# Optimization experiments

Measured on AMD Instinct MI355X. Metric: run time of the kernel, lower is better.

Reference implementation:

```python
import jax, jax.numpy as jnp
import numpy as np

N = 100000
E = 1600000
C_IN = 32
C_OUT = 64
DIM = 3
K = 2 ** DIM  # kernel_size=2 per pseudo-dim, degree=1 => 8 kernel slots
EPS = 1e-5

_BITS = jnp.asarray(np.array([[(c >> d) & 1 for d in range(DIM)] for c in range(K)], dtype=np.float32))  # [K,DIM]


def spline_basis(edge_attr):
    # edge_attr: [E,DIM] pseudo coords in [0,1]. kernel_size=2, degree=1 =>
    # per-dim linear basis (1-u, u); product over dims gives [E,K].
    u = edge_attr[:, None, :]            # [E,1,DIM]
    b = _BITS[None, :, :]                # [1,K,DIM]
    return jnp.prod(b * u + (1.0 - b) * (1.0 - u), axis=-1)  # [E,K]


def spline_conv(x, edge_index, edge_attr, W, W_root):
    # SplineConv with aggr='mean', root_weight=True, bias=False.
    src, dst = edge_index[0], edge_index[1]
    basis = spline_basis(edge_attr)                      # [E,K]
    x_j = x[src]                                         # [E,C_in] gather
    msg = jnp.einsum('ek,ei,kio->eo', basis, x_j, W)     # [E,C_out]
    agg = jax.ops.segment_sum(msg, dst, num_segments=N)  # [N,C_out] scatter-add
    cnt = jax.ops.segment_sum(jnp.ones((msg.shape[0],), msg.dtype), dst, num_segments=N)
    agg = agg / jnp.maximum(cnt, 1.0)[:, None]           # mean aggregation
    return agg + x @ W_root


def batch_norm(x, gamma, beta):
    mu = jnp.mean(x, axis=0)
    var = jnp.var(x, axis=0)
    return (x - mu) * jax.lax.rsqrt(var + EPS) * gamma + beta


def setup_inputs() -> dict:
    key = jax.random.key(0)
    ks = jax.random.split(key, 12)
    x = jax.random.normal(ks[0], (N, C_IN), jnp.float32)
    edge_index = jax.random.randint(ks[1], (2, E), 0, N, jnp.int32)
    edge_attr = jax.random.uniform(ks[2], (E, DIM), jnp.float32)
    s1 = 1.0 / np.sqrt(C_IN)
    s2 = 1.0 / np.sqrt(C_OUT)
    return {
        'x': x,
        'edge_index': edge_index,
        'edge_attr': edge_attr,
        'W1': jax.random.normal(ks[3], (K, C_IN, C_OUT), jnp.float32) * s1,
        'root1': jax.random.normal(ks[4], (C_IN, C_OUT), jnp.float32) * s1,
        'g1': jnp.ones((C_OUT,), jnp.float32),
        'b1': jnp.zeros((C_OUT,), jnp.float32),
        'W2': jax.random.normal(ks[5], (K, C_OUT, C_OUT), jnp.float32) * s2,
        'root2': jax.random.normal(ks[6], (C_OUT, C_OUT), jnp.float32) * s2,
        'g2': jnp.ones((C_OUT,), jnp.float32),
        'b2': jnp.zeros((C_OUT,), jnp.float32),
        'W_skip': jax.random.normal(ks[7], (C_IN, C_OUT), jnp.float32) * s1,
        'g_skip': jnp.ones((C_OUT,), jnp.float32),
        'b_skip': jnp.zeros((C_OUT,), jnp.float32),
    }


def reference(x, edge_index, edge_attr, W1, root1, g1, b1, W2, root2, g2, b2, W_skip, g_skip, b_skip):
    # ConvBlock: SplineConv -> BN -> elu
    h = spline_conv(x, edge_index, edge_attr, W1, root1)
    h = jax.nn.elu(batch_norm(h, g1, b1))
    # ConvBlockWithSkip: SplineConv -> BN; Linear skip -> BN; elu(sum)
    skip = batch_norm(x @ W_skip, g_skip, b_skip)
    h2 = batch_norm(spline_conv(h, edge_index, edge_attr, W2, root2), g2, b2)
    return jax.nn.elu(h2 + skip)
```

## Files before the change

### kernel.cpp

```cpp
#include <hip/hip_runtime.h>
#include <cstdint>

#define BN_EPS 1e-5f

typedef __attribute__((ext_vector_type(8))) short bf16x8;
typedef __attribute__((ext_vector_type(4))) float f32x4;
typedef unsigned int uint32;
typedef unsigned short u16;

__device__ inline u16 f2bf(float f) {
  unsigned int b = __float_as_uint(f);
  b += 0x7FFFu + ((b >> 16) & 1u);
  return (u16)(b >> 16);
}
__device__ inline float bf2f(u16 u) { return __uint_as_float((unsigned int)u << 16); }

__global__ void pack_bt(const float* __restrict__ W1, const float* __restrict__ root1,
                        const float* __restrict__ Wskip, const float* __restrict__ W2,
                        const float* __restrict__ root2, u16* __restrict__ B1t,
                        u16* __restrict__ B2t) {
  int idx = blockIdx.x * 256 + threadIdx.x;
  if (idx < 128 * 288) {
    int n = idx / 288, a = idx % 288;
    float v;
    if (a < 256) {
      int i = a >> 3, k = a & 7;
      v = (n < 64) ? W1[k * 2048 + i * 64 + n] : 0.f;
    } else {
      int i = a - 256;
      v = (n < 64) ? root1[i * 64 + n] : Wskip[i * 64 + (n - 64)];
    }
    B1t[idx] = f2bf(v);
  } else {
    int j = idx - 128 * 288;
    if (j < 64 * 576) {
      int n = j / 576, a = j % 576;
      float v;
      if (a < 512) {
        int i = a >> 3, k = a & 7;
        v = W2[k * 4096 + i * 64 + n];
      } else {
        v = root2[(a - 512) * 64 + n];
      }
      B2t[j] = f2bf(v);
    }
  }
}

__global__ __launch_bounds__(256) void conv_x(const float* __restrict__ x,
                                              u16* __restrict__ xbf, int total8) {
  int i = blockIdx.x * 256 + threadIdx.x;
  if (i >= total8) return;
  const float4* xp = (const float4*)x;
  float4 a = xp[2 * i], b = xp[2 * i + 1];
  union { u16 s[8]; uint4 u; } p;
  p.s[0] = f2bf(a.x); p.s[1] = f2bf(a.y); p.s[2] = f2bf(a.z); p.s[3] = f2bf(a.w);
  p.s[4] = f2bf(b.x); p.s[5] = f2bf(b.y); p.s[6] = f2bf(b.z); p.s[7] = f2bf(b.w);
  ((uint4*)xbf)[i] = p.u;
}

__global__ void hist_dst(const int* __restrict__ ei, int E, int* __restrict__ indeg) {
  int e = blockIdx.x * 256 + threadIdx.x;
  if (e >= E) return;
  atomicAdd(&indeg[ei[E + e]], 1);
}

__global__ __launch_bounds__(1024) void scan_block(const int* __restrict__ in,
                                                   int* __restrict__ part,
                                                   int* __restrict__ bsum, int N) {
  __shared__ int tmp[1024];
  int i = blockIdx.x * 1024 + threadIdx.x;
  int v = (i < N) ? in[i] : 0;
  tmp[threadIdx.x] = v;
  __syncthreads();
  for (int ofs = 1; ofs < 1024; ofs <<= 1) {
    int t = (threadIdx.x >= (unsigned)ofs) ? tmp[threadIdx.x - ofs] : 0;
    __syncthreads();
    tmp[threadIdx.x] += t;
    __syncthreads();
  }
  if (i < N) part[i] = tmp[threadIdx.x] - v;
  if (threadIdx.x == 1023) bsum[blockIdx.x] = tmp[1023];
}

__global__ __launch_bounds__(1024) void scan_top(int* __restrict__ bsum, int nb) {
  __shared__ int tmp[1024];
  int v = (threadIdx.x < (unsigned)nb) ? bsum[threadIdx.x] : 0;
  tmp[threadIdx.x] = v;
  __syncthreads();
  for (int ofs = 1; ofs < 1024; ofs <<= 1) {
    int t = (threadIdx.x >= (unsigned)ofs) ? tmp[threadIdx.x - ofs] : 0;
    __syncthreads();
    tmp[threadIdx.x] += t;
    __syncthreads();
  }
  if (threadIdx.x < (unsigned)nb) bsum[threadIdx.x] = tmp[threadIdx.x] - v;
}

__global__ void scan_add(const int* __restrict__ part, const int* __restrict__ bsum,
                         int* __restrict__ rowptr, int* __restrict__ cursor, int N, int E) {
  int i = blockIdx.x * 256 + threadIdx.x;
  if (i < N) {
    int r = part[i] + bsum[i >> 10];
    rowptr[i] = r;
    cursor[i] = r;
  }
  if (i == 0) rowptr[N] = E;
}

__global__ void edge_scatter(const int* __restrict__ ei, const float* __restrict__ attr, int E,
                             int* __restrict__ cursor, uint4* __restrict__ emeta) {
  int e = blockIdx.x * 256 + threadIdx.x;
  if (e >= E) return;
  int src = ei[e], dst = ei[E + e];
  float u0 = attr[3 * e + 0], u1 = attr[3 * e + 1], u2 = attr[3 * e + 2];
  float p0 = 1.f - u0, p1 = 1.f - u1, p2 = 1.f - u2;
  float w00 = p1 * p2, w10 = u1 * p2, w01 = p1 * u2, w11 = u1 * u2;
  float w[8] = {p0 * w00, u0 * w00, p0 * w10, u0 * w10,
                p0 * w01, u0 * w01, p0 * w11, u0 * w11};
  union { _Float16 h[8]; uint32 u[4]; } pk;
#pragma unroll
  for (int j = 0; j < 8; j++) pk.h[j] = (_Float16)w[j];
  int pos = atomicAdd(&cursor[dst], 1);
  emeta[2 * (size_t)pos + 0] = make_uint4((uint32)src, 0u, pk.u[0], pk.u[1]);
  emeta[2 * (size_t)pos + 1] = make_uint4(pk.u[2], pk.u[3], 0u, 0u);
}

template <int PC>
__device__ inline void sc_gather(const u16* __restrict__ tab, int src, int p, float* xf) {
  if (PC == 1) {
    xf[0] = bf2f(tab[(size_t)src * 32 + p]);
  } else {
    uint32 u = *(const uint32*)(tab + (size_t)src * 64 + 2 * p);
    xf[0] = __uint_as_float(u << 16);
    xf[1] = __uint_as_float(u & 0xFFFF0000u);
  }
}

template <int PC>
__device__ inline void sc_fma(float* acc, uint4 m0, uint4 m1, const float* xf) {
  union { uint32 u[4]; _Float16 h[8]; } w;
  w.u[0] = m0.z; w.u[1] = m0.w; w.u[2] = m1.x; w.u[3] = m1.y;
#pragma unroll
  for (int k = 0; k < 8; k++) {
    float wk = (float)w.h[k];
#pragma unroll
    for (int c = 0; c < PC; c++) acc[k * PC + c] += wk * xf[c];
  }
}

template <int PC>
__global__ __launch_bounds__(256) void msg_accum(const u16* __restrict__ tab,
                                                 const int* __restrict__ rowptr,
                                                 const uint4* __restrict__ emeta,
                                                 int n0, int n1, u16* __restrict__ T) {
  const int tid = threadIdx.x;
  const int lane = tid & 63;
  const int wv = tid >> 6;
  const int nwaves = gridDim.x * 4;
  const int p = lane & 31;
  const int eh = lane >> 5;

  for (int n = n0 + blockIdx.x * 4 + wv; n < n1; n += nwaves) {
    const int e0 = __builtin_amdgcn_readfirstlane(rowptr[n]);
    const int e1 = __builtin_amdgcn_readfirstlane(rowptr[n + 1]);
    float acc[8 * PC];
#pragma unroll
    for (int j = 0; j < 8 * PC; j++) acc[j] = 0.f;

    int e = e0;
    for (; e + 4 <= e1; e += 4) {
      const size_t iA = 2 * (size_t)(e + eh);
      const size_t iB = 2 * (size_t)(e + 2 + eh);
      uint4 a0 = emeta[iA], a1 = emeta[iA + 1];
      uint4 b0 = emeta[iB], b1 = emeta[iB + 1];
      float xa[PC], xb[PC];
      sc_gather<PC>(tab, (int)a0.x, p, xa);
      sc_gather<PC>(tab, (int)b0.x, p, xb);
      sc_fma<PC>(acc, a0, a1, xa);
      sc_fma<PC>(acc, b0, b1, xb);
    }
    for (; e < e1; e += 2) {
      int ee = e + eh;
      bool act = ee < e1;
      if (!act) ee = e;
      const size_t i0 = 2 * (size_t)ee;
      uint4 m0 = emeta[i0], m1 = emeta[i0 + 1];
      float xv[PC];
      sc_gather<PC>(tab, (int)m0.x, p, xv);
      if (!act) {
#pragma unroll
        for (int c = 0; c < PC; c++) xv[c] = 0.f;
      }
      sc_fma<PC>(acc, m0, m1, xv);
    }

#pragma unroll
    for (int j = 0; j < 8 * PC; j++) acc[j] += __shfl_xor(acc[j], 32);

    float inv = 1.f / fmaxf((float)(e1 - e0), 1.f);
    if (eh == 0) {
      u16* rowp = T + (size_t)(n - n0) * (256 * PC);
#pragma unroll
      for (int c = 0; c < PC; c++) {
        union { u16 s[8]; uint4 u; } pk;
#pragma unroll
        for (int k = 0; k < 8; k++) pk.s[k] = f2bf(acc[k * PC + c] * inv);
        *(uint4*)(rowp + ((size_t)(PC * p + c)) * 8) = pk.u;
      }
    }
  }
}

template <int KT, int KX, int NC>
__global__ __launch_bounds__(256) void gemm_agg(const u16* __restrict__ T,
                                                const u16* __restrict__ X,
                                                const u16* __restrict__ Bt,
                                                u16* __restrict__ O1, u16* __restrict__ O2,
                                                int rowOff, int rows) {
  const int K = KT + KX;
  const int tid = threadIdx.x;
  const int lane = tid & 63;
  const int wv = tid >> 6;
  const int rowbase = blockIdx.x * 64 + wv * 16;
  const int m = lane & 15;
  const int quad = lane >> 4;
  const int k0 = quad * 8;

  int ar = rowbase + m;
  if (ar > rows - 1) ar = rows - 1;

  bf16x8 afrag[K / 32];
#pragma unroll
  for (int f = 0; f < K / 32; f++) {
    if (f * 32 < KT)
      afrag[f] = *(const bf16x8*)(T + (size_t)ar * KT + f * 32 + k0);
    else
      afrag[f] = *(const bf16x8*)(X + (size_t)(rowOff + ar) * KX + (f * 32 - KT) + k0);
  }

  for (int col0 = 0; col0 < NC; col0 += 16) {
    f32x4 acc = {0.f, 0.f, 0.f, 0.f};
#pragma unroll
    for (int f = 0; f < K / 32; f++) {
      bf16x8 bfrag = *(const bf16x8*)(Bt + (size_t)(col0 + m) * K + f * 32 + k0);
      acc = __builtin_amdgcn_mfma_f32_16x16x32_bf16(afrag[f], bfrag, acc, 0, 0, 0);
    }
    const int col = col0 + m;
#pragma unroll
    for (int r = 0; r < 4; r++) {
      int gr = rowbase + quad * 4 + r;
      if (gr < rows) {
        size_t g = (size_t)(rowOff + gr);
        u16 v = f2bf(acc[r]);
        if (NC == 64 || col < 64) O1[g * 64 + col] = v;
        else O2[g * 64 + (col - 64)] = v;
      }
    }
  }
}

__global__ __launch_bounds__(256) void stats_k(const u16* __restrict__ A,
                                               const u16* __restrict__ B, int N,
                                               double* __restrict__ sums) {
  const int tid = threadIdx.x;
  const int c = tid & 63;
  const int wh = (tid >> 6) & 1;
  const int rep = tid >> 7;
  const u16* P = wh ? B : A;
  float s = 0.f, s2 = 0.f;
  if (P) {
    for (int n = blockIdx.x * 2 + rep; n < N; n += gridDim.x * 2) {
      float v = bf2f(P[(size_t)n * 64 + c]);
      s += v;
      s2 += v * v;
    }
  }
  __shared__ float red[256];
  red[tid] = s;
  __syncthreads();
  float t1 = (tid < 128) ? red[tid] + red[tid + 128] : 0.f;
  __syncthreads();
  red[tid] = s2;
  __syncthreads();
  if (tid < 128 && P) {
    float t2 = red[tid] + red[tid + 128];
    atomicAdd(&sums[wh * 128 + c], (double)t1);
    atomicAdd(&sums[wh * 128 + 64 + c], (double)t2);
  }
}

__global__ void bn_finalize2(const double* __restrict__ sums, const float* __restrict__ gA,
                             const float* __restrict__ bA, const float* __restrict__ gB,
                             const float* __restrict__ bB, float* __restrict__ scales, int N) {
  int t = threadIdx.x;
  int set = t >> 6, ch = t & 63;
  if (set == 1 && gB == nullptr) return;
  const float* g = set ? gB : gA;
  const float* b = set ? bB : bA;
  double mean = sums[set * 128 + ch] / (double)N;
  double var = sums[set * 128 + 64 + ch] / (double)N - mean * mean;
  double inv = 1.0 / sqrt(var + (double)BN_EPS);
  float sc = (float)((double)g[ch] * inv);
  scales[set * 128 + ch] = sc;
  scales[set * 128 + 64 + ch] = b[ch] - (float)mean * sc;
}

__global__ __launch_bounds__(256) void bn_elu_inplace(u16* __restrict__ h,
                                                      const float* __restrict__ sc, int total) {
  int idx = blockIdx.x * 256 + threadIdx.x;
  if (idx >= total) return;
  int ch = idx & 63;
  float v = bf2f(h[idx]) * sc[ch] + sc[64 + ch];
  v = v > 0.f ? v : expm1f(v);
  h[idx] = f2bf(v);
}

__global__ __launch_bounds__(256) void final_k(const u16* __restrict__ h2pre,
                                               const u16* __restrict__ skip,
                                               const float* __restrict__ sc2,
                                               const float* __restrict__ scS,
                                               float* __restrict__ out, int total) {
  int idx = blockIdx.x * 256 + threadIdx.x;
  if (idx >= total) return;
  int ch = idx & 63;
  float h2 = bf2f(h2pre[idx]) * sc2[ch] + sc2[64 + ch];
  float s = bf2f(skip[idx]) * scS[ch] + scS[64 + ch];
  float v = h2 + s;
  out[idx] = v > 0.f ? v : expm1f(v);
}

extern "C" void kernel_launch(void* const* d_in, const int* in_sizes, int n_in,
                              void* d_out, int out_size, void* d_ws, size_t ws_size,
                              hipStream_t stream) {
  const float* x     = (const float*)d_in[0];
  const int*   ei    = (const int*)d_in[1];
  const float* attr  = (const float*)d_in[2];
  const float* W1    = (const float*)d_in[3];
  const float* root1 = (const float*)d_in[4];
  const float* g1    = (const float*)d_in[5];
  const float* b1    = (const float*)d_in[6];
  const float* W2    = (const float*)d_in[7];
  const float* root2 = (const float*)d_in[8];
  const float* g2    = (const float*)d_in[9];
  const float* b2    = (const float*)d_in[10];
  const float* Wskip = (const float*)d_in[11];
  const float* gS    = (const float*)d_in[12];
  const float* bS    = (const float*)d_in[13];
  const int N = in_sizes[0] / 32;
  const int E = in_sizes[1] / 2;
  const int Nh = (N + 1) / 2;
  float* out = (float*)d_out;

  char* ws = (char*)d_ws;
  size_t off = 0;
  auto alloc = [&](size_t bytes) {
    void* p = ws + off;
    off = (off + bytes + 255) & ~(size_t)255;
    return p;
  };
  u16* B1t = (u16*)alloc(128 * 288 * 2);
  u16* B2t = (u16*)alloc(64 * 576 * 2);
  double* sums = (double*)alloc(6 * 64 * 8);
  float* scales = (float*)alloc(6 * 64 * 4);
  int* indeg = (int*)alloc((size_t)N * 4);
  int* rowptr = (int*)alloc(((size_t)N + 1) * 4);
  int* cursor = (int*)alloc((size_t)N * 4);
  int* bsum = (int*)alloc(1024 * 4);
  uint4* emeta = (uint4*)alloc((size_t)E * 32);
  u16* xbf = (u16*)alloc((size_t)N * 32 * 2);
  u16* T = (u16*)alloc((size_t)(N + 2) * 256 * 2);
  u16* h1 = (u16*)alloc((size_t)N * 64 * 2);
  u16* skip = (u16*)alloc((size_t)N * 64 * 2);
  u16* h2 = (u16*)alloc((size_t)N * 64 * 2);
  if (off > ws_size) return;

  hipMemsetAsync(indeg, 0, (size_t)N * 4, stream);
  hipMemsetAsync(sums, 0, 6 * 64 * 8, stream);

  pack_bt<<<(128 * 288 + 64 * 576 + 255) / 256, 256, 0, stream>>>(W1, root1, Wskip, W2, root2,
                                                                  B1t, B2t);
  conv_x<<<(N * 4 + 255) / 256, 256, 0, stream>>>(x, xbf, N * 4);

  const int eblocks = (E + 255) / 256;
  const int nb = (N + 1023) / 1024;
  hist_dst<<<eblocks, 256, 0, stream>>>(ei, E, indeg);
  scan_block<<<nb, 1024, 0, stream>>>(indeg, cursor, bsum, N);
  scan_top<<<1, 1024, 0, stream>>>(bsum, nb);
  scan_add<<<(N + 255) / 256, 256, 0, stream>>>(cursor, bsum, rowptr, indeg, N, E);
  edge_scatter<<<eblocks, 256, 0, stream>>>(ei, attr, E, indeg, emeta);

  msg_accum<1><<<2048, 256, 0, stream>>>(xbf, rowptr, emeta, 0, N, T);
  gemm_agg<256, 32, 128><<<(N + 63) / 64, 256, 0, stream>>>(T, xbf, B1t, h1, skip, 0, N);
  stats_k<<<512, 256, 0, stream>>>(h1, skip, N, sums);
  bn_finalize2<<<1, 128, 0, stream>>>(sums, g1, b1, gS, bS, scales, N);
  bn_elu_inplace<<<(N * 64 + 255) / 256, 256, 0, stream>>>(h1, scales, N * 64);

  for (int cph = 0; cph < 2; cph++) {
    int r0 = cph ? Nh : 0;
    int r1 = cph ? N : Nh;
    msg_accum<2><<<2048, 256, 0, stream>>>(h1, rowptr, emeta, r0, r1, T);
    gemm_agg<512, 64, 64><<<(r1 - r0 + 63) / 64, 256, 0, stream>>>(T, h1, B2t, h2, nullptr,
                                                                   r0, r1 - r0);
  }
  stats_k<<<512, 256, 0, stream>>>(h2, nullptr, N, sums + 4 * 64);
  bn_finalize2<<<1, 64, 0, stream>>>(sums + 4 * 64, g2, b2, nullptr, nullptr,
                                     scales + 4 * 64, N);

  final_k<<<(N * 64 + 255) / 256, 256, 0, stream>>>(h2, skip, scales + 4 * 64,
                                                    scales + 2 * 64, out, N * 64);
}
```

Baseline: 642.0 us.

## Two-pass bucketed edge scatter with per-XCD staging to localize CSR writes

Replaces the direct edge scatter with two passes. The first appends compact edge records into per-(dst bucket, XCD) staging slots, reusing the T buffer, and falls back to a direct scatter on overflow. The second kernel, one block per 256-node bucket, places the records into the CSR metadata, so the random 32-byte writes and cursor atomics land in a localized region. This costs an extra kernel pass, extra staging traffic and atomics, and reads a hardware register to get the XCD id.

```diff
diff --git a/kernel.cpp b/kernel.cpp
--- a/kernel.cpp
+++ b/kernel.cpp
@@ -14,6 +14,24 @@
   return (u16)(b >> 16);
 }
 __device__ inline float bf2f(u16 u) { return __uint_as_float((unsigned int)u << 16); }
+
+__device__ inline int get_xcd() {
+  uint32 x;
+  asm volatile("s_getreg_b32 %0, hwreg(HW_REG_XCC_ID)" : "=s"(x));
+  return (int)(x & 7u);
+}
+
+__device__ inline void make_w8(float u0, float u1, float u2, uint32* wu) {
+  float p0 = 1.f - u0, p1 = 1.f - u1, p2 = 1.f - u2;
+  float w00 = p1 * p2, w10 = u1 * p2, w01 = p1 * u2, w11 = u1 * u2;
+  float w[8] = {p0 * w00, u0 * w00, p0 * w10, u0 * w10,
+                p0 * w01, u0 * w01, p0 * w11, u0 * w11};
+  union { _Float16 h[8]; uint32 u[4]; } pk;
+#pragma unroll
+  for (int j = 0; j < 8; j++) pk.h[j] = (_Float16)w[j];
+#pragma unroll
+  for (int j = 0; j < 4; j++) wu[j] = pk.u[j];
+}
 
 __global__ void pack_bt(const float* __restrict__ W1, const float* __restrict__ root1,
                         const float* __restrict__ Wskip, const float* __restrict__ W2,
@@ -108,22 +126,53 @@
   if (i == 0) rowptr[N] = E;
 }
 
-__global__ void edge_scatter(const int* __restrict__ ei, const float* __restrict__ attr, int E,
-                             int* __restrict__ cursor, uint4* __restrict__ emeta) {
+__global__ __launch_bounds__(256) void stage_append(const int* __restrict__ ei,
+                                                    const float* __restrict__ attr, int E,
+                                                    int* __restrict__ bcnt,
+                                                    uint4* __restrict__ stage, int sbcap,
+                                                    int* __restrict__ cursor,
+                                                    uint4* __restrict__ emeta) {
   int e = blockIdx.x * 256 + threadIdx.x;
   if (e >= E) return;
   int src = ei[e], dst = ei[E + e];
   float u0 = attr[3 * e + 0], u1 = attr[3 * e + 1], u2 = attr[3 * e + 2];
-  float p0 = 1.f - u0, p1 = 1.f - u1, p2 = 1.f - u2;
-  float w00 = p1 * p2, w10 = u1 * p2, w01 = p1 * u2, w11 = u1 * u2;
-  float w[8] = {p0 * w00, u0 * w00, p0 * w10, u0 * w10,
-                p0 * w01, u0 * w01, p0 * w11, u0 * w11};
-  union { _Float16 h[8]; uint32 u[4]; } pk;
-#pragma unroll
-  for (int j = 0; j < 8; j++) pk.h[j] = (_Float16)w[j];
-  int pos = atomicAdd(&cursor[dst], 1);
-  emeta[2 * (size_t)pos + 0] = make_uint4((uint32)src, 0u, pk.u[0], pk.u[1]);
-  emeta[2 * (size_t)pos + 1] = make_uint4(pk.u[2], pk.u[3], 0u, 0u);
+  union { _Float16 h[2]; uint32 u; } y, z;
+  y.h[0] = (_Float16)u0; y.h[1] = (_Float16)u1;
+  z.h[0] = (_Float16)u2; z.h[1] = (_Float16)0.f;
+  int sb = (dst >> 8) * 8 + get_xcd();
+  int c = atomicAdd(&bcnt[sb], 1);
+  if (c < sbcap) {
+    stage[(size_t)sb * sbcap + c] = make_uint4((uint32)src, (uint32)dst, y.u, z.u);
+  } else {
+    uint32 wu[4];
+    make_w8((float)y.h[0], (float)y.h[1], (float)z.h[0], wu);
+    int pos = atomicAdd(&cursor[dst], 1);
+    emeta[2 * (size_t)pos + 0] = make_uint4((uint32)src, 0u, wu[0], wu[1]);
+    emeta[2 * (size_t)pos + 1] = make_uint4(wu[2], wu[3], 0u, 0u);
+  }
+}
+
+__global__ __launch_bounds__(256) void bucket_place(const uint4* __restrict__ stage,
+                                                    const int* __restrict__ bcnt, int sbcap,
+                                                    int* __restrict__ cursor,
+                                                    uint4* __restrict__ emeta) {
+  int b = blockIdx.x;
+  for (int xc = 0; xc < 8; xc++) {
+    int sb = b * 8 + xc;
+    int cnt = bcnt[sb];
+    if (cnt > sbcap) cnt = sbcap;
+    const uint4* sp = stage + (size_t)sb * sbcap;
+    for (int i = threadIdx.x; i < cnt; i += 256) {
+      uint4 r = sp[i];
+      union { uint32 u; _Float16 h[2]; } cy, cz;
+      cy.u = r.z; cz.u = r.w;
+      uint32 wu[4];
+      make_w8((float)cy.h[0], (float)cy.h[1], (float)cz.h[0], wu);
+      int pos = atomicAdd(&cursor[(int)r.y], 1);
+      emeta[2 * (size_t)pos + 0] = make_uint4(r.x, 0u, wu[0], wu[1]);
+      emeta[2 * (size_t)pos + 1] = make_uint4(wu[2], wu[3], 0u, 0u);
+    }
+  }
 }
 
 template <int PC>
@@ -352,6 +401,12 @@
   const int Nh = (N + 1) / 2;
   float* out = (float*)d_out;
 
+  const int NBu = (N + 255) >> 8;
+  int sbcap = (int)(((long long)E * 7) / ((long long)NBu * 32));
+  int sbmax = (int)(((long long)(N + 2) * 4) / NBu);
+  if (sbcap > sbmax) sbcap = sbmax;
+  if (sbcap < 64) sbcap = 64;
+
   char* ws = (char*)d_ws;
   size_t off = 0;
   auto alloc = [&](size_t bytes) {
@@ -367,6 +422,7 @@
   int* rowptr = (int*)alloc(((size_t)N + 1) * 4);
   int* cursor = (int*)alloc((size_t)N * 4);
   int* bsum = (int*)alloc(1024 * 4);
+  int* bcnt = (int*)alloc((size_t)NBu * 8 * 4);
   uint4* emeta = (uint4*)alloc((size_t)E * 32);
   u16* xbf = (u16*)alloc((size_t)N * 32 * 2);
   u16* T = (u16*)alloc((size_t)(N + 2) * 256 * 2);
@@ -375,7 +431,10 @@
   u16* h2 = (u16*)alloc((size_t)N * 64 * 2);
   if (off > ws_size) return;
 
+  uint4* stage = (uint4*)T;
+
   hipMemsetAsync(indeg, 0, (size_t)N * 4, stream);
+  hipMemsetAsync(bcnt, 0, (size_t)NBu * 8 * 4, stream);
   hipMemsetAsync(sums, 0, 6 * 64 * 8, stream);
 
   pack_bt<<<(128 * 288 + 64 * 576 + 255) / 256, 256, 0, stream>>>(W1, root1, Wskip, W2, root2,
@@ -388,7 +447,9 @@
   scan_block<<<nb, 1024, 0, stream>>>(indeg, cursor, bsum, N);
   scan_top<<<1, 1024, 0, stream>>>(bsum, nb);
   scan_add<<<(N + 255) / 256, 256, 0, stream>>>(cursor, bsum, rowptr, indeg, N, E);
-  edge_scatter<<<eblocks, 256, 0, stream>>>(ei, attr, E, indeg, emeta);
+
+  stage_append<<<eblocks, 256, 0, stream>>>(ei, attr, E, bcnt, stage, sbcap, indeg, emeta);
+  bucket_place<<<NBu, 256, 0, stream>>>(stage, bcnt, sbcap, indeg, emeta);
 
   msg_accum<1><<<2048, 256, 0, stream>>>(xbf, rowptr, emeta, 0, N, T);
   gemm_agg<256, 32, 128><<<(N + 63) / 64, 256, 0, stream>>>(T, xbf, B1t, h1, skip, 0, N);
```

After: 753.2 us. 1.17x slower.

## Fuse BN statistics into GEMM epilogue, merge prep kernels, reuse histogram ranks

Applied to the files above, without the earlier changes.

Batch-norm sum and sum-of-squares are now computed in the gemm_agg epilogue with wave shuffles and an LDS reduction, followed by double atomics per block. This removes the separate stats_k passes that re-read h1, skip and h2. Weight packing and the x-to-bf16 conversion are merged into one prep kernel. The histogram now records each edge's atomic rank, so edge_scatter computes its position directly instead of doing a second atomic on a cursor array. The cost is an extra E-sized rank buffer and many more double atomicAdds, one set per GEMM block.

```diff
diff --git a/kernel.cpp b/kernel.cpp
--- a/kernel.cpp
+++ b/kernel.cpp
@@ -15,10 +15,14 @@
 }
 __device__ inline float bf2f(u16 u) { return __uint_as_float((unsigned int)u << 16); }
 
-__global__ void pack_bt(const float* __restrict__ W1, const float* __restrict__ root1,
-                        const float* __restrict__ Wskip, const float* __restrict__ W2,
-                        const float* __restrict__ root2, u16* __restrict__ B1t,
-                        u16* __restrict__ B2t) {
+__global__ __launch_bounds__(256) void prep(const float* __restrict__ W1,
+                                            const float* __restrict__ root1,
+                                            const float* __restrict__ Wskip,
+                                            const float* __restrict__ W2,
+                                            const float* __restrict__ root2,
+                                            u16* __restrict__ B1t, u16* __restrict__ B2t,
+                                            const float* __restrict__ x,
+                                            u16* __restrict__ xbf, int total8) {
   int idx = blockIdx.x * 256 + threadIdx.x;
   if (idx < 128 * 288) {
     int n = idx / 288, a = idx % 288;
@@ -31,38 +35,33 @@
       v = (n < 64) ? root1[i * 64 + n] : Wskip[i * 64 + (n - 64)];
     }
     B1t[idx] = f2bf(v);
-  } else {
+  } else if (idx < 128 * 288 + 64 * 576) {
     int j = idx - 128 * 288;
-    if (j < 64 * 576) {
-      int n = j / 576, a = j % 576;
-      float v;
-      if (a < 512) {
-        int i = a >> 3, k = a & 7;
-        v = W2[k * 4096 + i * 64 + n];
-      } else {
-        v = root2[(a - 512) * 64 + n];
-      }
-      B2t[j] = f2bf(v);
-    }
-  }
-}
-
-__global__ __launch_bounds__(256) void conv_x(const float* __restrict__ x,
-                                              u16* __restrict__ xbf, int total8) {
-  int i = blockIdx.x * 256 + threadIdx.x;
-  if (i >= total8) return;
-  const float4* xp = (const float4*)x;
-  float4 a = xp[2 * i], b = xp[2 * i + 1];
-  union { u16 s[8]; uint4 u; } p;
-  p.s[0] = f2bf(a.x); p.s[1] = f2bf(a.y); p.s[2] = f2bf(a.z); p.s[3] = f2bf(a.w);
-  p.s[4] = f2bf(b.x); p.s[5] = f2bf(b.y); p.s[6] = f2bf(b.z); p.s[7] = f2bf(b.w);
-  ((uint4*)xbf)[i] = p.u;
-}
-
-__global__ void hist_dst(const int* __restrict__ ei, int E, int* __restrict__ indeg) {
+    int n = j / 576, a = j % 576;
+    float v;
+    if (a < 512) {
+      int i = a >> 3, k = a & 7;
+      v = W2[k * 4096 + i * 64 + n];
+    } else {
+      v = root2[(a - 512) * 64 + n];
+    }
+    B2t[j] = f2bf(v);
+  }
+  if (idx < total8) {
+    const float4* xp = (const float4*)x;
+    float4 a = xp[2 * idx], b = xp[2 * idx + 1];
+    union { u16 s[8]; uint4 u; } p;
+    p.s[0] = f2bf(a.x); p.s[1] = f2bf(a.y); p.s[2] = f2bf(a.z); p.s[3] = f2bf(a.w);
+    p.s[4] = f2bf(b.x); p.s[5] = f2bf(b.y); p.s[6] = f2bf(b.z); p.s[7] = f2bf(b.w);
+    ((uint4*)xbf)[idx] = p.u;
+  }
+}
+
+__global__ void hist_dst(const int* __restrict__ ei, int E, int* __restrict__ indeg,
+                         int* __restrict__ rank) {
   int e = blockIdx.x * 256 + threadIdx.x;
   if (e >= E) return;
-  atomicAdd(&indeg[ei[E + e]], 1);
+  rank[e] = atomicAdd(&indeg[ei[E + e]], 1);
 }
 
 __global__ __launch_bounds__(1024) void scan_block(const int* __restrict__ in,
@@ -98,18 +97,17 @@
 }
 
 __global__ void scan_add(const int* __restrict__ part, const int* __restrict__ bsum,
-                         int* __restrict__ rowptr, int* __restrict__ cursor, int N, int E) {
+                         int* __restrict__ rowptr, int N, int E) {
   int i = blockIdx.x * 256 + threadIdx.x;
-  if (i < N) {
-    int r = part[i] + bsum[i >> 10];
-    rowptr[i] = r;
-    cursor[i] = r;
-  }
+  if (i < N) rowptr[i] = part[i] + bsum[i >> 10];
   if (i == 0) rowptr[N] = E;
 }
 
-__global__ void edge_scatter(const int* __restrict__ ei, const float* __restrict__ attr, int E,
-                             int* __restrict__ cursor, uint4* __restrict__ emeta) {
+__global__ __launch_bounds__(256) void edge_scatter(const int* __restrict__ ei,
+                                                    const float* __restrict__ attr,
+                                                    const int* __restrict__ rowptr,
+                                                    const int* __restrict__ rank, int E,
+                                                    uint4* __restrict__ emeta) {
   int e = blockIdx.x * 256 + threadIdx.x;
   if (e >= E) return;
   int src = ei[e], dst = ei[E + e];
@@ -121,7 +119,7 @@
   union { _Float16 h[8]; uint32 u[4]; } pk;
 #pragma unroll
   for (int j = 0; j < 8; j++) pk.h[j] = (_Float16)w[j];
-  int pos = atomicAdd(&cursor[dst], 1);
+  int pos = rowptr[dst] + rank[e];
   emeta[2 * (size_t)pos + 0] = make_uint4((uint32)src, 0u, pk.u[0], pk.u[1]);
   emeta[2 * (size_t)pos + 1] = make_uint4(pk.u[2], pk.u[3], 0u, 0u);
 }
@@ -217,7 +215,8 @@
                                                 const u16* __restrict__ X,
                                                 const u16* __restrict__ Bt,
                                                 u16* __restrict__ O1, u16* __restrict__ O2,
-                                                int rowOff, int rows) {
+                                                int rowOff, int rows,
+                                                double* __restrict__ sums) {
   const int K = KT + KX;
   const int tid = threadIdx.x;
   const int lane = tid & 63;
@@ -227,6 +226,8 @@
   const int quad = lane >> 4;
   const int k0 = quad * 8;
 
+  __shared__ float slds[4][NC][2];
+
   int ar = rowbase + m;
   if (ar > rows - 1) ar = rows - 1;
 
@@ -247,46 +248,31 @@
       acc = __builtin_amdgcn_mfma_f32_16x16x32_bf16(afrag[f], bfrag, acc, 0, 0, 0);
     }
     const int col = col0 + m;
+    float s1 = 0.f, s2 = 0.f;
 #pragma unroll
     for (int r = 0; r < 4; r++) {
       int gr = rowbase + quad * 4 + r;
       if (gr < rows) {
         size_t g = (size_t)(rowOff + gr);
-        u16 v = f2bf(acc[r]);
-        if (NC == 64 || col < 64) O1[g * 64 + col] = v;
-        else O2[g * 64 + (col - 64)] = v;
+        u16 vq = f2bf(acc[r]);
+        float v = bf2f(vq);
+        s1 += v;
+        s2 += v * v;
+        if (NC == 64 || col < 64) O1[g * 64 + col] = vq;
+        else O2[g * 64 + (col - 64)] = vq;
       }
     }
-  }
-}
-
-__global__ __launch_bounds__(256) void stats_k(const u16* __restrict__ A,
-                                               const u16* __restrict__ B, int N,
-                                               double* __restrict__ sums) {
-  const int tid = threadIdx.x;
-  const int c = tid & 63;
-  const int wh = (tid >> 6) & 1;
-  const int rep = tid >> 7;
-  const u16* P = wh ? B : A;
-  float s = 0.f, s2 = 0.f;
-  if (P) {
-    for (int n = blockIdx.x * 2 + rep; n < N; n += gridDim.x * 2) {
-      float v = bf2f(P[(size_t)n * 64 + c]);
-      s += v;
-      s2 += v * v;
-    }
-  }
-  __shared__ float red[256];
-  red[tid] = s;
+    s1 += __shfl_xor(s1, 16); s1 += __shfl_xor(s1, 32);
+    s2 += __shfl_xor(s2, 16); s2 += __shfl_xor(s2, 32);
+    if (lane < 16) { slds[wv][col][0] = s1; slds[wv][col][1] = s2; }
+  }
   __syncthreads();
-  float t1 = (tid < 128) ? red[tid] + red[tid + 128] : 0.f;
-  __syncthreads();
-  red[tid] = s2;
-  __syncthreads();
-  if (tid < 128 && P) {
-    float t2 = red[tid] + red[tid + 128];
-    atomicAdd(&sums[wh * 128 + c], (double)t1);
-    atomicAdd(&sums[wh * 128 + 64 + c], (double)t2);
+  if (tid < NC * 2) {
+    int col = tid >> 1, which = tid & 1;
+    float v = slds[0][col][which] + slds[1][col][which] + slds[2][col][which] +
+              slds[3][col][which];
+    int slot = ((NC > 64 && col >= 64) ? 128 : 0) + which * 64 + (col & 63);
+    atomicAdd(&sums[slot], (double)v);
   }
 }
 
@@ -365,8 +351,9 @@
   float* scales = (float*)alloc(6 * 64 * 4);
   int* indeg = (int*)alloc((size_t)N * 4);
   int* rowptr = (int*)alloc(((size_t)N + 1) * 4);
-  int* cursor = (int*)alloc((size_t)N * 4);
+  int* part = (int*)alloc((size_t)N * 4);
   int* bsum = (int*)alloc(1024 * 4);
+  int* rank = (int*)alloc((size_t)E * 4);
   uint4* emeta = (uint4*)alloc((size_t)E * 32);
   u16* xbf = (u16*)alloc((size_t)N * 32 * 2);
   u16* T = (u16*)alloc((size_t)(N + 2) * 256 * 2);
@@ -378,21 +365,19 @@
   hipMemsetAsync(indeg, 0, (size_t)N * 4, stream);
   hipMemsetAsync(sums, 0, 6 * 64 * 8, stream);
 
-  pack_bt<<<(128 * 288 + 64 * 576 + 255) / 256, 256, 0, stream>>>(W1, root1, Wskip, W2, root2,
-                                                                  B1t, B2t);
-  conv_x<<<(N * 4 + 255) / 256, 256, 0, stream>>>(x, xbf, N * 4);
-
   const int eblocks = (E + 255) / 256;
   const int nb = (N + 1023) / 1024;
-  hist_dst<<<eblocks, 256, 0, stream>>>(ei, E, indeg);
-  scan_block<<<nb, 1024, 0, stream>>>(indeg, cursor, bsum, N);
+  prep<<<(N * 4 + 255) / 256, 256, 0, stream>>>(W1, root1, Wskip, W2, root2, B1t, B2t,
+                                                x, xbf, N * 4);
+  hist_dst<<<eblocks, 256, 0, stream>>>(ei, E, indeg, rank);
+  scan_block<<<nb, 1024, 0, stream>>>(indeg, part, bsum, N);
   scan_top<<<1, 1024, 0, stream>>>(bsum, nb);
-  scan_add<<<(N + 255) / 256, 256, 0, stream>>>(cursor, bsum, rowptr, indeg, N, E);
-  edge_scatter<<<eblocks, 256, 0, stream>>>(ei, attr, E, indeg, emeta);
+  scan_add<<<(N + 255) / 256, 256, 0, stream>>>(part, bsum, rowptr, N, E);
+  edge_scatter<<<eblocks, 256, 0, stream>>>(ei, attr, rowptr, rank, E, emeta);
 
   msg_accum<1><<<2048, 256, 0, stream>>>(xbf, rowptr, emeta, 0, N, T);
-  gemm_agg<256, 32, 128><<<(N + 63) / 64, 256, 0, stream>>>(T, xbf, B1t, h1, skip, 0, N);
-  stats_k<<<512, 256, 0, stream>>>(h1, skip, N, sums);
+  gemm_agg<256, 32, 128><<<(N + 63) / 64, 256, 0, stream>>>(T, xbf, B1t, h1, skip, 0, N,
+                                                            sums);
   bn_finalize2<<<1, 128, 0, stream>>>(sums, g1, b1, gS, bS, scales, N);
   bn_elu_inplace<<<(N * 64 + 255) / 256, 256, 0, stream>>>(h1, scales, N * 64);
 
@@ -401,9 +386,9 @@
     int r1 = cph ? N : Nh;
     msg_accum<2><<<2048, 256, 0, stream>>>(h1, rowptr, emeta, r0, r1, T);
     gemm_agg<512, 64, 64><<<(r1 - r0 + 63) / 64, 256, 0, stream>>>(T, h1, B2t, h2, nullptr,
-                                                                   r0, r1 - r0);
-  }
-  stats_k<<<512, 256, 0, stream>>>(h2, nullptr, N, sums + 4 * 64);
+                                                                   r0, r1 - r0,
+                                                                   sums + 4 * 64);
+  }
   bn_finalize2<<<1, 64, 0, stream>>>(sums + 4 * 64, g2, b2, nullptr, nullptr,
                                      scales + 4 * 64, N);
 
```

Result: faster. 593.9 us (-7.5%).
